# Kernel tuning notes

Hardware: AMD Instinct MI355X
Metric: run time of the kernel (lower is better)

The kernel has to match this reference:

```python
import jax, jax.numpy as jnp
import numpy as np

N, D, S, K = 4096, 256, 32, 4   # nodes, in_dim(=out_dim), subspace_dim, num_heads
ETA = 0.5
LAMBDA_SPARSE = 0.05
EDGE_P = 0.02  # graph density for the random adjacency mask


def setup_inputs() -> dict:
    key = jax.random.key(0)
    k1, k2, k3 = jax.random.split(key, 3)
    H = jax.random.normal(k1, (N, D), dtype=jnp.float32)
    # binary adjacency mask with self-loops, stored as float (matches torch usage)
    mask = (jax.random.uniform(k2, (N, N)) < EDGE_P).astype(jnp.float32)
    adj_mask = jnp.maximum(mask, jnp.eye(N, dtype=jnp.float32))
    # per-head orthonormal subspace bases U[k] = qr(randn(D,S)) -> [K, D, S]
    raw = jax.random.normal(k3, (K, D, S), dtype=jnp.float32)
    U, _ = jnp.linalg.qr(raw)
    log_precision = jnp.zeros((K, S), dtype=jnp.float32)
    threshold = jnp.full((D,), LAMBDA_SPARSE, dtype=jnp.float32)
    return {"H": H, "adj_mask": adj_mask, "U": U,
            "log_precision": log_precision, "threshold": threshold}


def reference(H, adj_mask, U, log_precision, threshold):
    s = U.shape[-1]
    inv_sqrt_s = 1.0 / jnp.sqrt(jnp.asarray(s, dtype=H.dtype))
    neg = (1.0 - adj_mask) * (-1e9)  # [N, N] additive mask

    # scan over heads keeps peak memory at one [N,N] score matrix at a time
    def head_step(agg, xs):
        Uk, lpk = xs                       # [D,S], [S]
        Z = H @ Uk                         # [N,S]  (= Zk^T in the torch code)
        Zs = Z * jnp.exp(lpk)              # precision-scaled
        scores = (Zs @ Z.T) * inv_sqrt_s + neg   # [N,N]
        alpha = jax.nn.softmax(scores, axis=-1)
        agg = agg + (alpha @ Z) @ Uk.T     # [N,D] == (Uk @ (Zk @ alpha^T))^T
        return agg, None

    agg, _ = jax.lax.scan(head_step, jnp.zeros_like(H), (U, log_precision))
    H_half = H + ETA * agg                 # in_dim == out_dim -> no proj

    # soft threshold
    H_out = jnp.sign(H_half) * jax.nn.relu(jnp.abs(H_half) - threshold[None, :])

    # orthogonality loss: sum_k ||Uk^T Uk - I||_F^2 + sum_{k<l} ||Uk^T Ul||_F^2
    C = jnp.einsum('kda,ldb->klab', U, U)  # [K,K,S,S] gram blocks (K,S small)
    Kh = U.shape[0]
    I = jnp.eye(s, dtype=U.dtype)
    diag_blocks = C[jnp.arange(Kh), jnp.arange(Kh)]          # [K,S,S]
    orth_loss = ((diag_blocks - I) ** 2).sum()
    upper = jnp.triu(jnp.ones((Kh, Kh), dtype=U.dtype), 1)[:, :, None, None]
    orth_loss = orth_loss + ((C ** 2) * upper).sum()
    return H_out, orth_loss
```

## Files before the change

### kernel.cpp

```cpp
#include <hip/hip_runtime.h>
#include <math.h>

constexpr int NN = 4096;
constexpr int DD = 256;
constexpr int SS = 32;
constexpr int KK = 4;
constexpr int MAXN = 192;
constexpr float ETA = 0.5f;

#define MEMFENCE() __asm__ volatile("" ::: "memory")

__global__ __launch_bounds__(256) void prep_kernel(
    const float* __restrict__ H, const float* __restrict__ U,
    const float* __restrict__ lp, const float* __restrict__ mask,
    float* __restrict__ Z, float* __restrict__ elp, float* __restrict__ lossp,
    int* __restrict__ nbr_g, int* __restrict__ cnt_g) {
  const int tid = threadIdx.x;

  if (blockIdx.x < 1024) {
    __shared__ float Hl[16][DD];
    const int k = blockIdx.x & 3;
    const int n0 = (blockIdx.x >> 2) * 16;

    const float4* H4 = (const float4*)(H + (size_t)n0 * DD);
    float4* Hl4 = (float4*)&Hl[0][0];
    for (int i = tid; i < 16 * DD / 4; i += 256) Hl4[i] = H4[i];
    __syncthreads();

    const int s = tid & 31;
    const int n_l = (tid >> 5) & 7;
    const float* Uk = U + (size_t)k * DD * SS;
    float acc0 = 0.f, acc1 = 0.f;
#pragma unroll 4
    for (int dq = 0; dq < DD / 4; dq++) {
      const float4 h0 = Hl4[n_l * (DD / 4) + dq];
      const float4 h1 = Hl4[(n_l + 8) * (DD / 4) + dq];
      const float u0 = Uk[(4 * dq + 0) * SS + s];
      const float u1 = Uk[(4 * dq + 1) * SS + s];
      const float u2 = Uk[(4 * dq + 2) * SS + s];
      const float u3 = Uk[(4 * dq + 3) * SS + s];
      acc0 += h0.x * u0 + h0.y * u1 + h0.z * u2 + h0.w * u3;
      acc1 += h1.x * u0 + h1.y * u1 + h1.z * u2 + h1.w * u3;
    }
    Z[((size_t)k * NN + n0 + n_l) * SS + s] = acc0;
    Z[((size_t)k * NN + n0 + n_l + 8) * SS + s] = acc1;
  } else if (blockIdx.x < 2048) {
    const int wv = tid >> 6;
    const int lane = tid & 63;
    const int row = (blockIdx.x - 1024) * 4 + wv;
    const float4* m4 = (const float4*)(mask + (size_t)row * NN);
    const unsigned long long lt = (1ULL << lane) - 1ULL;
    int* out = nbr_g + (size_t)row * MAXN;
    int cnt = 0;
#pragma unroll 4
    for (int it = 0; it < 16; it++) {
      const int i = it * 64 + lane;
      const float4 v = m4[i];
      unsigned long long b;
      b = __ballot(v.x > 0.5f);
      if (v.x > 0.5f) { const int p = cnt + (int)__popcll(b & lt); if (p < MAXN) out[p] = 4 * i; }
      cnt += (int)__popcll(b);
      b = __ballot(v.y > 0.5f);
      if (v.y > 0.5f) { const int p = cnt + (int)__popcll(b & lt); if (p < MAXN) out[p] = 4 * i + 1; }
      cnt += (int)__popcll(b);
      b = __ballot(v.z > 0.5f);
      if (v.z > 0.5f) { const int p = cnt + (int)__popcll(b & lt); if (p < MAXN) out[p] = 4 * i + 2; }
      cnt += (int)__popcll(b);
      b = __ballot(v.w > 0.5f);
      if (v.w > 0.5f) { const int p = cnt + (int)__popcll(b & lt); if (p < MAXN) out[p] = 4 * i + 3; }
      cnt += (int)__popcll(b);
    }
    if (lane == 0) cnt_g[row] = min(cnt, MAXN);
  } else {
    __shared__ float red[4];
    const int pair = blockIdx.x - 2048;
    if (pair == 0 && tid < KK * SS) elp[tid] = expf(lp[tid]);
    const int pk[10] = {0, 0, 0, 0, 1, 1, 1, 2, 2, 3};
    const int pl[10] = {0, 1, 2, 3, 1, 2, 3, 2, 3, 3};
    const int k = pk[pair], l = pl[pair];
    const int b = tid & 31;
    const int a0 = tid >> 5;
    float acc[4] = {0.f, 0.f, 0.f, 0.f};
    for (int d = 0; d < DD; d++) {
      const float ub = U[((size_t)l * DD + d) * SS + b];
#pragma unroll
      for (int j = 0; j < 4; j++)
        acc[j] += U[((size_t)k * DD + d) * SS + a0 + 8 * j] * ub;
    }
    float tot = 0.f;
#pragma unroll
    for (int j = 0; j < 4; j++) {
      const float cv = acc[j] - ((k == l && (a0 + 8 * j) == b) ? 1.0f : 0.0f);
      tot += cv * cv;
    }
#pragma unroll
    for (int off = 32; off >= 1; off >>= 1) tot += __shfl_xor(tot, off);
    if ((tid & 63) == 0) red[tid >> 6] = tot;
    __syncthreads();
    if (tid == 0) lossp[pair] = red[0] + red[1] + red[2] + red[3];
  }
}

__global__ __launch_bounds__(256) void attn_row(
    const float* __restrict__ Z, const float* __restrict__ elp,
    const float* __restrict__ lossp, const int* __restrict__ nbr_g,
    const int* __restrict__ cnt_g, float* __restrict__ AO,
    float* __restrict__ loss) {
  const int tid = threadIdx.x;
  const int wv = tid >> 6;
  const int lane = tid & 63;
  const int row = blockIdx.x;

  __shared__ float scw[4][MAXN];

  if (blockIdx.x == 0 && tid == 0) {
    float t = 0.f;
#pragma unroll
    for (int i = 0; i < 10; i++) t += lossp[i];
    loss[0] = t;
  }

  const int c = cnt_g[row];
  const int* nb = nbr_g + (size_t)row * MAXN;

  const int k = wv;
  const int p_sub = lane >> 3;
  const int sq = lane & 7;
  const float inv_sqrt_s = 0.17677669529663687f;
  const float* Zk = Z + (size_t)k * NN * SS;

  float4 q4;
  {
    const float4 a = ((const float4*)(Z + ((size_t)k * NN + row) * SS))[sq];
    const float4 e = ((const float4*)(elp + k * SS))[sq];
    q4.x = a.x * e.x; q4.y = a.y * e.y; q4.z = a.z * e.z; q4.w = a.w * e.w;
  }

  float lmax = -3.0e38f;
  for (int p0 = 0; p0 < c; p0 += 16) {
    const int pa = p0 + p_sub;
    const int pb = pa + 8;
    const bool aA = pa < c, aB = pb < c;
    float4 zA = {0.f, 0.f, 0.f, 0.f}, zB = {0.f, 0.f, 0.f, 0.f};
    if (aA) zA = ((const float4*)(Zk + (size_t)nb[pa] * SS))[sq];
    if (aB) zB = ((const float4*)(Zk + (size_t)nb[pb] * SS))[sq];
    float dA = q4.x * zA.x + q4.y * zA.y + q4.z * zA.z + q4.w * zA.w;
    float dB = q4.x * zB.x + q4.y * zB.y + q4.z * zB.z + q4.w * zB.w;
    dA += __shfl_xor(dA, 1); dB += __shfl_xor(dB, 1);
    dA += __shfl_xor(dA, 2); dB += __shfl_xor(dB, 2);
    dA += __shfl_xor(dA, 4); dB += __shfl_xor(dB, 4);
    dA = aA ? dA * inv_sqrt_s : -3.0e38f;
    dB = aB ? dB * inv_sqrt_s : -3.0e38f;
    if (sq == 0 && aA) scw[wv][pa] = dA;
    if (sq == 0 && aB) scw[wv][pb] = dB;
    lmax = fmaxf(lmax, fmaxf(dA, dB));
  }
  MEMFENCE();
#pragma unroll
  for (int off = 32; off >= 1; off >>= 1) lmax = fmaxf(lmax, __shfl_xor(lmax, off));

  float wsum = 0.f;
#pragma unroll
  for (int t = 0; t < 3; t++) {
    const int p = lane + t * 64;
    if (p < c) {
      const float w = __expf(scw[wv][p] - lmax);
      scw[wv][p] = w;
      wsum += w;
    }
  }
  MEMFENCE();
#pragma unroll
  for (int off = 32; off >= 1; off >>= 1) wsum += __shfl_xor(wsum, off);
  const float invl = 1.0f / wsum;

  float4 o4 = {0.f, 0.f, 0.f, 0.f};
  for (int p0 = 0; p0 < c; p0 += 16) {
    const int pa = p0 + p_sub;
    const int pb = pa + 8;
    const bool aA = pa < c, aB = pb < c;
    float wA = 0.f, wB = 0.f;
    float4 zA = {0.f, 0.f, 0.f, 0.f}, zB = {0.f, 0.f, 0.f, 0.f};
    if (aA) { wA = scw[wv][pa]; zA = ((const float4*)(Zk + (size_t)nb[pa] * SS))[sq]; }
    if (aB) { wB = scw[wv][pb]; zB = ((const float4*)(Zk + (size_t)nb[pb] * SS))[sq]; }
    o4.x += wA * zA.x + wB * zB.x;
    o4.y += wA * zA.y + wB * zB.y;
    o4.z += wA * zA.z + wB * zB.z;
    o4.w += wA * zA.w + wB * zB.w;
  }
#pragma unroll
  for (int off = 8; off <= 32; off <<= 1) {
    o4.x += __shfl_xor(o4.x, off);
    o4.y += __shfl_xor(o4.y, off);
    o4.z += __shfl_xor(o4.z, off);
    o4.w += __shfl_xor(o4.w, off);
  }
  if (p_sub == 0) {
    float4 o;
    o.x = o4.x * invl; o.y = o4.y * invl; o.z = o4.z * invl; o.w = o4.w * invl;
    ((float4*)AO)[(size_t)row * (KK * SS / 4) + k * 8 + sq] = o;
  }
}

__global__ __launch_bounds__(256) void epilogue_kernel(
    const float* __restrict__ H, const float* __restrict__ U,
    const float* __restrict__ thr, const float* __restrict__ AO,
    float* __restrict__ Hout) {
  __shared__ float AOl[4][KK * SS];
  const int tid = threadIdx.x;
  const int r0 = blockIdx.x * 4;

  const float4* AO4 = (const float4*)(AO + (size_t)r0 * KK * SS);
  float4* AOl4 = (float4*)&AOl[0][0];
  if (tid < 128) AOl4[tid] = AO4[tid];
  __syncthreads();

  const int d = tid;
  float acc[4] = {0.f, 0.f, 0.f, 0.f};
  const float4* U4 = (const float4*)U;
#pragma unroll
  for (int k = 0; k < KK; k++) {
    const int ubase = (k * DD + d) * (SS / 4);
#pragma unroll
    for (int sq = 0; sq < SS / 4; sq++) {
      const float4 u = U4[ubase + sq];
#pragma unroll
      for (int r = 0; r < 4; r++) {
        const float4 a = AOl4[r * (KK * SS / 4) + k * (SS / 4) + sq];
        acc[r] += u.x * a.x + u.y * a.y + u.z * a.z + u.w * a.w;
      }
    }
  }
  const float tv = thr[d];
#pragma unroll
  for (int r = 0; r < 4; r++) {
    const float h = H[(size_t)(r0 + r) * DD + d] + ETA * acc[r];
    const float ab = fabsf(h) - tv;
    Hout[(size_t)(r0 + r) * DD + d] = (ab > 0.0f) ? copysignf(ab, h) : 0.0f;
  }
}

extern "C" void kernel_launch(void* const* d_in, const int* in_sizes, int n_in,
                              void* d_out, int out_size, void* d_ws, size_t ws_size,
                              hipStream_t stream) {
  const float* H    = (const float*)d_in[0];
  const float* mask = (const float*)d_in[1];
  const float* U    = (const float*)d_in[2];
  const float* lp   = (const float*)d_in[3];
  const float* thr  = (const float*)d_in[4];

  float* Hout = (float*)d_out;
  float* loss = Hout + (size_t)NN * DD;

  float* Z     = (float*)d_ws;
  float* AO    = Z + (size_t)KK * NN * SS;
  float* elp   = AO + (size_t)NN * KK * SS;
  float* lossp = elp + KK * SS;
  int*   nbr_g = (int*)(lossp + 16);
  int*   cnt_g = nbr_g + (size_t)NN * MAXN;

  prep_kernel<<<2058, 256, 0, stream>>>(H, U, lp, mask, Z, elp, lossp, nbr_g, cnt_g);
  attn_row<<<NN, 256, 0, stream>>>(Z, elp, lossp, nbr_g, cnt_g, AO, loss);
  epilogue_kernel<<<NN / 4, 256, 0, stream>>>(H, U, thr, AO, Hout);
}
```

Measured before the change: 171.0 us.

## Split mask row compaction across four waves per row with shared-memory merge

Each row's neighbor extraction now uses a whole block: four waves each scan a quarter of the mask row, compact into shared-memory segments, then write at prefix offsets. Previously one wave scanned an entire 4096-wide row serially. This shortens the serial ballot chain per row and raises memory-level parallelism when reading the 64 MB mask. The change also reorders blocks so mask rows launch first and raises the unroll of the Z projection loop. A risk is that a quarter-row segment holding more than 96 neighbors is truncated, which the old code would have kept up to 192.

```diff
diff --git a/kernel.cpp b/kernel.cpp
--- a/kernel.cpp
+++ b/kernel.cpp
@@ -6,6 +6,7 @@
 constexpr int SS = 32;
 constexpr int KK = 4;
 constexpr int MAXN = 192;
+constexpr int SEGMAX = 96;
 constexpr float ETA = 0.5f;
 
 #define MEMFENCE() __asm__ volatile("" ::: "memory")
@@ -17,10 +18,53 @@
     int* __restrict__ nbr_g, int* __restrict__ cnt_g) {
   const int tid = threadIdx.x;
 
-  if (blockIdx.x < 1024) {
+  if (blockIdx.x < 4096) {
+    __shared__ int segn[4][SEGMAX];
+    __shared__ int segc[4];
+    const int wv = tid >> 6;
+    const int lane = tid & 63;
+    const int row = blockIdx.x;
+
+    const float4* m4 = (const float4*)(mask + (size_t)row * NN);
+    const unsigned long long lt = (1ULL << lane) - 1ULL;
+    int cnt = 0;
+#pragma unroll
+    for (int it = 0; it < 4; it++) {
+      const int i = wv * 256 + it * 64 + lane;
+      const float4 v = m4[i];
+      unsigned long long b;
+      b = __ballot(v.x > 0.5f);
+      if (v.x > 0.5f) { const int p = cnt + (int)__popcll(b & lt); if (p < SEGMAX) segn[wv][p] = 4 * i; }
+      cnt += (int)__popcll(b);
+      b = __ballot(v.y > 0.5f);
+      if (v.y > 0.5f) { const int p = cnt + (int)__popcll(b & lt); if (p < SEGMAX) segn[wv][p] = 4 * i + 1; }
+      cnt += (int)__popcll(b);
+      b = __ballot(v.z > 0.5f);
+      if (v.z > 0.5f) { const int p = cnt + (int)__popcll(b & lt); if (p < SEGMAX) segn[wv][p] = 4 * i + 2; }
+      cnt += (int)__popcll(b);
+      b = __ballot(v.w > 0.5f);
+      if (v.w > 0.5f) { const int p = cnt + (int)__popcll(b & lt); if (p < SEGMAX) segn[wv][p] = 4 * i + 3; }
+      cnt += (int)__popcll(b);
+    }
+    if (lane == 0) segc[wv] = min(cnt, SEGMAX);
+    MEMFENCE();
+    __syncthreads();
+
+    const int c0 = segc[0], c1 = segc[1], c2 = segc[2], c3 = segc[3];
+    const int offs[4] = {0, c0, c0 + c1, c0 + c1 + c2};
+    int* out = nbr_g + (size_t)row * MAXN;
+    const int myc = segc[wv];
+    const int myoff = offs[wv];
+    for (int i = lane; i < myc; i += 64) {
+      const int p = myoff + i;
+      if (p < MAXN) out[p] = segn[wv][i];
+    }
+    if (tid == 0) cnt_g[row] = min(c0 + c1 + c2 + c3, MAXN);
+  } else if (blockIdx.x < 5120) {
     __shared__ float Hl[16][DD];
-    const int k = blockIdx.x & 3;
-    const int n0 = (blockIdx.x >> 2) * 16;
+    const int b = blockIdx.x - 4096;
+    const int k = b & 3;
+    const int n0 = (b >> 2) * 16;
 
     const float4* H4 = (const float4*)(H + (size_t)n0 * DD);
     float4* Hl4 = (float4*)&Hl[0][0];
@@ -31,7 +75,7 @@
     const int n_l = (tid >> 5) & 7;
     const float* Uk = U + (size_t)k * DD * SS;
     float acc0 = 0.f, acc1 = 0.f;
-#pragma unroll 4
+#pragma unroll 8
     for (int dq = 0; dq < DD / 4; dq++) {
       const float4 h0 = Hl4[n_l * (DD / 4) + dq];
       const float4 h1 = Hl4[(n_l + 8) * (DD / 4) + dq];
@@ -44,36 +88,9 @@
     }
     Z[((size_t)k * NN + n0 + n_l) * SS + s] = acc0;
     Z[((size_t)k * NN + n0 + n_l + 8) * SS + s] = acc1;
-  } else if (blockIdx.x < 2048) {
-    const int wv = tid >> 6;
-    const int lane = tid & 63;
-    const int row = (blockIdx.x - 1024) * 4 + wv;
-    const float4* m4 = (const float4*)(mask + (size_t)row * NN);
-    const unsigned long long lt = (1ULL << lane) - 1ULL;
-    int* out = nbr_g + (size_t)row * MAXN;
-    int cnt = 0;
-#pragma unroll 4
-    for (int it = 0; it < 16; it++) {
-      const int i = it * 64 + lane;
-      const float4 v = m4[i];
-      unsigned long long b;
-      b = __ballot(v.x > 0.5f);
-      if (v.x > 0.5f) { const int p = cnt + (int)__popcll(b & lt); if (p < MAXN) out[p] = 4 * i; }
-      cnt += (int)__popcll(b);
-      b = __ballot(v.y > 0.5f);
-      if (v.y > 0.5f) { const int p = cnt + (int)__popcll(b & lt); if (p < MAXN) out[p] = 4 * i + 1; }
-      cnt += (int)__popcll(b);
-      b = __ballot(v.z > 0.5f);
-      if (v.z > 0.5f) { const int p = cnt + (int)__popcll(b & lt); if (p < MAXN) out[p] = 4 * i + 2; }
-      cnt += (int)__popcll(b);
-      b = __ballot(v.w > 0.5f);
-      if (v.w > 0.5f) { const int p = cnt + (int)__popcll(b & lt); if (p < MAXN) out[p] = 4 * i + 3; }
-      cnt += (int)__popcll(b);
-    }
-    if (lane == 0) cnt_g[row] = min(cnt, MAXN);
   } else {
     __shared__ float red[4];
-    const int pair = blockIdx.x - 2048;
+    const int pair = blockIdx.x - 5120;
     if (pair == 0 && tid < KK * SS) elp[tid] = expf(lp[tid]);
     const int pk[10] = {0, 0, 0, 0, 1, 1, 1, 2, 2, 3};
     const int pl[10] = {0, 1, 2, 3, 1, 2, 3, 2, 3, 3};
@@ -259,7 +276,7 @@
   int*   nbr_g = (int*)(lossp + 16);
   int*   cnt_g = nbr_g + (size_t)NN * MAXN;
 
-  prep_kernel<<<2058, 256, 0, stream>>>(H, U, lp, mask, Z, elp, lossp, nbr_g, cnt_g);
+  prep_kernel<<<5130, 256, 0, stream>>>(H, U, lp, mask, Z, elp, lossp, nbr_g, cnt_g);
   attn_row<<<NN, 256, 0, stream>>>(Z, elp, lossp, nbr_g, cnt_g, AO, loss);
   epilogue_kernel<<<NN / 4, 256, 0, stream>>>(H, U, thr, AO, Hout);
 }
```

Result: no change. 172.0 us (+0.6%).
